# Kernel optimization log

Hardware: AMD Instinct MI355X
Metric: run time of the kernel (lower is better)

## Reference

```python
import jax, jax.numpy as jnp
from jax import lax
import numpy as np

H = 32  # hidden size (hardcoded by Linear(32,1) in the source)
I = 1   # input size

def setup_inputs() -> dict:
    key = jax.random.key(0)
    ks = jax.random.split(key, 8)
    B, T = 2048, 1024
    s_ih = 1.0 / np.sqrt(H)
    inp = {
        "x": jax.random.normal(ks[0], (B, T, I), dtype=jnp.float32),
        "h_state": jnp.zeros((1, B, H), dtype=jnp.float32),
        # GRU params, PyTorch layout: gates stacked as [r; z; n] -> [3H, *]
        "W_ih": jax.random.uniform(ks[1], (3 * H, I), jnp.float32, -s_ih, s_ih),
        "W_hh": jax.random.uniform(ks[2], (3 * H, H), jnp.float32, -s_ih, s_ih),
        "b_ih": jax.random.uniform(ks[3], (3 * H,), jnp.float32, -s_ih, s_ih),
        "b_hh": jax.random.uniform(ks[4], (3 * H,), jnp.float32, -s_ih, s_ih),
        # output Linear(32, 1)
        "W_out": jax.random.uniform(ks[5], (1, H), jnp.float32, -s_ih, s_ih),
        "b_out": jax.random.uniform(ks[6], (1,), jnp.float32, -s_ih, s_ih),
    }
    return inp

def _gru(x, h0, W_ih, W_hh, b_ih, b_hh):
    # Precompute input projections for all timesteps: [B,T,3H]
    x_proj = jnp.einsum('bti,gi->btg', x, W_ih) + b_ih
    xp_t = jnp.swapaxes(x_proj, 0, 1)  # [T,B,3H] for scan

    def step(h, xp):
        gh = h @ W_hh.T + b_hh  # [B,3H]
        r = jax.nn.sigmoid(xp[:, :H] + gh[:, :H])
        z = jax.nn.sigmoid(xp[:, H:2 * H] + gh[:, H:2 * H])
        n = jnp.tanh(xp[:, 2 * H:] + r * gh[:, 2 * H:])
        h_new = (1.0 - z) * n + z * h
        return h_new, h_new

    h_final, h_seq = lax.scan(step, h0[0], xp_t)
    return jnp.swapaxes(h_seq, 0, 1), h_final[None]  # [B,T,H], [1,B,H]

def reference(x, h_state, W_ih, W_hh, b_ih, b_hh, W_out, b_out):
    r_out, h_n = _gru(x, h_state, W_ih, W_hh, b_ih, b_hh)
    # per-timestep Linear(32,1), vectorized over time
    y = jnp.einsum('bth,oh->bto', r_out, W_out) + b_out  # [B,T,1]
    return (y, h_n)
```

## Files before the change

### kernel.cpp

```cpp
#include <hip/hip_runtime.h>


constexpr int H  = 32;
constexpr int TT = 1024;
constexpr int BB = 2048;

typedef _Float16 hf2 __attribute__((ext_vector_type(2)));

__device__ __forceinline__ unsigned pack2(float a, float b) {
    hf2 t; t.x = (_Float16)a; t.y = (_Float16)b;
    return __builtin_bit_cast(unsigned, t);
}

#define DOT48                                          \
    "v_dot2_f32_f16 v68, %[r0], v36, %[br]\n\t"        \
    "v_dot2_f32_f16 v69, %[z0], v36, %[bz]\n\t"        \
    "v_dot2_f32_f16 v70, %[n0], v36, %[bn]\n\t"        \
    "v_dot2_f32_f16 v68, %[r1], v37, v68\n\t"          \
    "v_dot2_f32_f16 v69, %[z1], v37, v69\n\t"          \
    "v_dot2_f32_f16 v70, %[n1], v37, v70\n\t"          \
    "v_dot2_f32_f16 v68, %[r2], v38, v68\n\t"          \
    "v_dot2_f32_f16 v69, %[z2], v38, v69\n\t"          \
    "v_dot2_f32_f16 v70, %[n2], v38, v70\n\t"          \
    "v_dot2_f32_f16 v68, %[r3], v39, v68\n\t"          \
    "v_dot2_f32_f16 v69, %[z3], v39, v69\n\t"          \
    "v_dot2_f32_f16 v70, %[n3], v39, v70\n\t"          \
    "v_dot2_f32_f16 v68, %[r4], v40, v68\n\t"          \
    "v_dot2_f32_f16 v69, %[z4], v40, v69\n\t"          \
    "v_dot2_f32_f16 v70, %[n4], v40, v70\n\t"          \
    "v_dot2_f32_f16 v68, %[r5], v41, v68\n\t"          \
    "v_dot2_f32_f16 v69, %[z5], v41, v69\n\t"          \
    "v_dot2_f32_f16 v70, %[n5], v41, v70\n\t"          \
    "v_dot2_f32_f16 v68, %[r6], v42, v68\n\t"          \
    "v_dot2_f32_f16 v69, %[z6], v42, v69\n\t"          \
    "v_dot2_f32_f16 v70, %[n6], v42, v70\n\t"          \
    "v_dot2_f32_f16 v68, %[r7], v43, v68\n\t"          \
    "v_dot2_f32_f16 v69, %[z7], v43, v69\n\t"          \
    "v_dot2_f32_f16 v70, %[n7], v43, v70\n\t"          \
    "v_dot2_f32_f16 v68, %[r8], v44, v68\n\t"          \
    "v_dot2_f32_f16 v69, %[z8], v44, v69\n\t"          \
    "v_dot2_f32_f16 v70, %[n8], v44, v70\n\t"          \
    "v_dot2_f32_f16 v68, %[r9], v45, v68\n\t"          \
    "v_dot2_f32_f16 v69, %[z9], v45, v69\n\t"          \
    "v_dot2_f32_f16 v70, %[n9], v45, v70\n\t"          \
    "v_dot2_f32_f16 v68, %[r10], v46, v68\n\t"         \
    "v_dot2_f32_f16 v69, %[z10], v46, v69\n\t"         \
    "v_dot2_f32_f16 v70, %[n10], v46, v70\n\t"         \
    "v_dot2_f32_f16 v68, %[r11], v47, v68\n\t"         \
    "v_dot2_f32_f16 v69, %[z11], v47, v69\n\t"         \
    "v_dot2_f32_f16 v70, %[n11], v47, v70\n\t"         \
    "v_dot2_f32_f16 v68, %[r12], v48, v68\n\t"         \
    "v_dot2_f32_f16 v69, %[z12], v48, v69\n\t"         \
    "v_dot2_f32_f16 v70, %[n12], v48, v70\n\t"         \
    "v_dot2_f32_f16 v68, %[r13], v49, v68\n\t"         \
    "v_dot2_f32_f16 v69, %[z13], v49, v69\n\t"         \
    "v_dot2_f32_f16 v70, %[n13], v49, v70\n\t"         \
    "v_dot2_f32_f16 v68, %[r14], v50, v68\n\t"         \
    "v_dot2_f32_f16 v69, %[z14], v50, v69\n\t"         \
    "v_dot2_f32_f16 v70, %[n14], v50, v70\n\t"         \
    "v_dot2_f32_f16 v68, %[r15], v51, v68\n\t"         \
    "v_dot2_f32_f16 v69, %[z15], v51, v69\n\t"         \
    "v_dot2_f32_f16 v70, %[n15], v51, v70\n\t"

#define TAIL(XREG, HREG)                               \
    "v_fmac_f32 v68, " XREG ", %[wir]\n\t"             \
    "v_fmac_f32 v69, " XREG ", %[wiz]\n\t"             \
    "v_exp_f32 v71, v68\n\t"                           \
    "v_exp_f32 v72, v69\n\t"                           \
    "v_fma_f32 v74, " XREG ", %[wi], %[bi]\n\t"        \
    "s_nop 3\n\t"                                      \
    "v_add_f32 v71, 1.0, v71\n\t"                      \
    "v_add_f32 v72, 1.0, v72\n\t"                      \
    "v_rcp_f32 v71, v71\n\t"                           \
    "v_rcp_f32 v72, v72\n\t"                           \
    "s_nop 3\n\t"                                      \
    "v_fmac_f32 v74, v71, v70\n\t"                     \
    "v_exp_f32 v75, v74\n\t"                           \
    "s_nop 3\n\t"                                      \
    "v_add_f32 v75, 1.0, v75\n\t"                      \
    "v_rcp_f32 v75, v75\n\t"                           \
    "s_nop 3\n\t"                                      \
    "v_fma_f32 v76, -2.0, v75, 1.0\n\t"                \
    "v_sub_f32 v77, " HREG ", v76\n\t"                 \
    "v_fma_f32 " HREG ", v72, v77, v76\n\t"

__global__ __launch_bounds__(256, 1)
void gru_fused(const float* __restrict__ x,
               const float* __restrict__ h0,
               const float* __restrict__ W_ih,
               const float* __restrict__ W_hh,
               const float* __restrict__ b_ih,
               const float* __restrict__ b_hh,
               const float* __restrict__ W_out,
               const float* __restrict__ b_out,
               float* __restrict__ out)
{
    __shared__ __align__(16) _Float16 hbuf[4][64];
    __shared__ __align__(8) float xstage[4][2][36];
    __shared__ float ybuf[4][2][33 * 32];

    const int tid  = threadIdx.x;
    const int w    = tid >> 6;
    const int lane = tid & 63;
    const int half = lane >> 5;
    const int j    = lane & 31;
    const int gw   = (blockIdx.x << 2) | w;
    const int b    = (gw << 1) | half;

    const float NL2E = -1.44269504f;
    const float P2L2 =  2.88539008f;

    const float* Wrp = &W_hh[(0 * H + j) * H];
    const float* Wzp = &W_hh[(1 * H + j) * H];
    const float* Wnp = &W_hh[(2 * H + j) * H];
    unsigned wr[16], wz[16], wn[16];
#pragma unroll
    for (int k = 0; k < 16; ++k) {
        wr[k] = pack2(Wrp[2 * k] * NL2E, Wrp[2 * k + 1] * NL2E);
        wz[k] = pack2(Wzp[2 * k] * NL2E, Wzp[2 * k + 1] * NL2E);
        wn[k] = pack2(Wnp[2 * k] * P2L2, Wnp[2 * k + 1] * P2L2);
    }
    const float wir = W_ih[j] * NL2E;
    const float wiz = W_ih[H + j] * NL2E;
    const float br  = (b_ih[j] + b_hh[j]) * NL2E;
    const float bz  = (b_ih[H + j] + b_hh[H + j]) * NL2E;
    const float bhn = b_hh[2 * H + j] * P2L2;
    const float win = W_ih[2 * H + j] * P2L2;
    const float bin = b_ih[2 * H + j] * P2L2;
    const float wo  = W_out[j];
    const float bo  = b_out[0];

    float h = h0[b * H + j];

    const float* xb = x + (size_t)b * TT;
    float*       yb = out + (size_t)b * TT;

    const unsigned ha = (unsigned)(size_t)&hbuf[w][half * 32 + j];
    const unsigned hr = (unsigned)(size_t)&hbuf[w][half * 32];
    const unsigned xw = (unsigned)(size_t)&xstage[w][half][j];
    const unsigned xa = (unsigned)(size_t)&xstage[w][half][0];
    const unsigned ya = (unsigned)(size_t)&ybuf[w][half][j];
    const float* yr = &ybuf[w][half][0];

#pragma unroll 1
    for (int t0 = 0; t0 < TT; t0 += 32) {
        const float xv = xb[t0 + j];

        asm volatile(
            "s_mov_b32 s20, 16\n\t"
            "v_mov_b32 v82, %[ya]\n\t"
            "v_mov_b32 v83, %[xa]\n\t"
            "ds_write_b32 %[xw], %[xv]\n\t"
            "ds_read_b64 v[80:81], v83\n\t"
            "v_cvt_f16_f32 v33, %[h]\n\t"
            "ds_write_b16 %[ha], v33\n\t"
            "ds_read_b128 v[36:39], %[hr]\n\t"
            "ds_read_b128 v[40:43], %[hr] offset:16\n\t"
            "ds_read_b128 v[44:47], %[hr] offset:32\n\t"
            "ds_read_b128 v[48:51], %[hr] offset:48\n\t"
            "ds_write_b32 v82, v78\n\t"

            "L_gru_%=:\n\t"
            "s_waitcnt lgkmcnt(1)\n\t"
            DOT48
            TAIL("v80", "%[h]")
            "v_cvt_f16_f32 v33, %[h]\n\t"
            "ds_write_b16 %[ha], v33\n\t"
            "ds_read_b128 v[36:39], %[hr]\n\t"
            "ds_read_b128 v[40:43], %[hr] offset:16\n\t"
            "ds_read_b128 v[44:47], %[hr] offset:32\n\t"
            "ds_read_b128 v[48:51], %[hr] offset:48\n\t"
            "v_mul_f32 v78, %[wo], %[h]\n\t"
            "ds_write_b32 v82, v78\n\t"
            "s_waitcnt lgkmcnt(1)\n\t"
            DOT48
            TAIL("v81", "%[h]")
            "v_cvt_f16_f32 v33, %[h]\n\t"
            "ds_write_b16 %[ha], v33\n\t"
            "ds_read_b128 v[36:39], %[hr]\n\t"
            "ds_read_b128 v[40:43], %[hr] offset:16\n\t"
            "ds_read_b128 v[44:47], %[hr] offset:32\n\t"
            "ds_read_b128 v[48:51], %[hr] offset:48\n\t"
            "ds_read_b64 v[80:81], v83 offset:8\n\t"
            "v_mul_f32 v78, %[wo], %[h]\n\t"
            "ds_write_b32 v82, v78 offset:132\n\t"
            "v_add_u32 v82, 264, v82\n\t"
            "v_add_u32 v83, 8, v83\n\t"
            "s_sub_i32 s20, s20, 1\n\t"
            "s_cmp_gt_i32 s20, 0\n\t"
            "s_cbranch_scc1 L_gru_%=\n\t"
            "s_waitcnt lgkmcnt(0)"
            : [h]"+v"(h)
            : [xv]"v"(xv), [ha]"v"(ha), [hr]"v"(hr), [xw]"v"(xw), [xa]"v"(xa),
              [ya]"v"(ya),
              [wir]"v"(wir), [wiz]"v"(wiz), [wi]"v"(win), [bi]"v"(bin),
              [wo]"v"(wo), [br]"v"(br), [bz]"v"(bz), [bn]"v"(bhn),
              [r0]"v"(wr[0]), [r1]"v"(wr[1]), [r2]"v"(wr[2]), [r3]"v"(wr[3]),
              [r4]"v"(wr[4]), [r5]"v"(wr[5]), [r6]"v"(wr[6]), [r7]"v"(wr[7]),
              [r8]"v"(wr[8]), [r9]"v"(wr[9]), [r10]"v"(wr[10]), [r11]"v"(wr[11]),
              [r12]"v"(wr[12]), [r13]"v"(wr[13]), [r14]"v"(wr[14]), [r15]"v"(wr[15]),
              [z0]"v"(wz[0]), [z1]"v"(wz[1]), [z2]"v"(wz[2]), [z3]"v"(wz[3]),
              [z4]"v"(wz[4]), [z5]"v"(wz[5]), [z6]"v"(wz[6]), [z7]"v"(wz[7]),
              [z8]"v"(wz[8]), [z9]"v"(wz[9]), [z10]"v"(wz[10]), [z11]"v"(wz[11]),
              [z12]"v"(wz[12]), [z13]"v"(wz[13]), [z14]"v"(wz[14]), [z15]"v"(wz[15]),
              [n0]"v"(wn[0]), [n1]"v"(wn[1]), [n2]"v"(wn[2]), [n3]"v"(wn[3]),
              [n4]"v"(wn[4]), [n5]"v"(wn[5]), [n6]"v"(wn[6]), [n7]"v"(wn[7]),
              [n8]"v"(wn[8]), [n9]"v"(wn[9]), [n10]"v"(wn[10]), [n11]"v"(wn[11]),
              [n12]"v"(wn[12]), [n13]"v"(wn[13]), [n14]"v"(wn[14]), [n15]"v"(wn[15])
            : "memory", "scc", "s20",
              "v33", "v36", "v37", "v38", "v39", "v40", "v41", "v42", "v43",
              "v44", "v45", "v46", "v47", "v48", "v49", "v50", "v51",
              "v68", "v69", "v70", "v71", "v72", "v74", "v75", "v76", "v77",
              "v78", "v80", "v81", "v82", "v83");

        float s0 = 0.0f, s1 = 0.0f, s2 = 0.0f, s3 = 0.0f;
#pragma unroll
        for (int k = 0; k < 32; k += 4) {
            s0 += yr[33 * j + k + 0];
            s1 += yr[33 * j + k + 1];
            s2 += yr[33 * j + k + 2];
            s3 += yr[33 * j + k + 3];
        }
        yb[t0 + j] = (s0 + s1) + (s2 + s3) + bo;
        __builtin_amdgcn_wave_barrier();
    }

    out[(size_t)BB * TT + b * H + j] = h;

#undef DOT48
#undef TAIL
}

extern "C" void kernel_launch(void* const* d_in, const int* in_sizes, int n_in,
                              void* d_out, int out_size, void* d_ws, size_t ws_size,
                              hipStream_t stream) {
    const float* x     = (const float*)d_in[0];
    const float* h0    = (const float*)d_in[1];
    const float* W_ih  = (const float*)d_in[2];
    const float* W_hh  = (const float*)d_in[3];
    const float* b_ih  = (const float*)d_in[4];
    const float* b_hh  = (const float*)d_in[5];
    const float* W_out = (const float*)d_in[6];
    const float* b_out = (const float*)d_in[7];
    float* out = (float*)d_out;

    dim3 grid(BB / 8);
    dim3 block(256);
    gru_fused<<<grid, block, 0, stream>>>(x, h0, W_ih, W_hh, b_ih, b_hh,
                                          W_out, b_out, out);
}
```

Measured before the change: 287.6 us.

## Broadcast hidden state via permlane16 swap and DPP butterflies instead of LDS

Each timestep's hidden-state exchange among the 32 lanes of a batch row used to go through an LDS write and four 128-bit LDS reads. It now uses v_permlane16_swap plus a set of DPP quad_perm and mirror moves to build the 16 packed f16 operands in registers. The W_hh weights are permuted per lane to match the butterfly ordering, and a runtime probe detects how the swap behaves. This removes LDS latency and waitcnt from the serial recurrence critical path, at the cost of many extra VALU moves and s_nop hazard stalls per step.

```diff
diff --git a/kernel.cpp b/kernel.cpp
--- a/kernel.cpp
+++ b/kernel.cpp
@@ -84,6 +84,34 @@
     "v_sub_f32 v77, " HREG ", v76\n\t"                 \
     "v_fma_f32 " HREG ", v72, v77, v76\n\t"
 
+#define BFLY(F1, F2)                                                        \
+    "v_cvt_f16_f32 v33, %[h]\n\t"                                           \
+    "v_mov_b32 v34, v33\n\t"                                                \
+    F1                                                                      \
+    "s_nop 1\n\t"                                                           \
+    "v_permlane16_swap_b32 v33, v34\n\t"                                    \
+    F2                                                                      \
+    "s_nop 1\n\t"                                                           \
+    "v_pack_b32_f16 v36, v33, v34\n\t"                                      \
+    "s_nop 1\n\t"                                                           \
+    "v_mov_b32 v37, v36 quad_perm:[1,0,3,2] row_mask:0xf bank_mask:0xf\n\t" \
+    "s_nop 1\n\t"                                                           \
+    "v_mov_b32 v38, v36 quad_perm:[2,3,0,1] row_mask:0xf bank_mask:0xf\n\t" \
+    "v_mov_b32 v39, v37 quad_perm:[2,3,0,1] row_mask:0xf bank_mask:0xf\n\t" \
+    "s_nop 1\n\t"                                                           \
+    "v_mov_b32 v40, v36 row_half_mirror row_mask:0xf bank_mask:0xf\n\t"     \
+    "v_mov_b32 v41, v37 row_half_mirror row_mask:0xf bank_mask:0xf\n\t"     \
+    "v_mov_b32 v42, v38 row_half_mirror row_mask:0xf bank_mask:0xf\n\t"     \
+    "v_mov_b32 v43, v39 row_half_mirror row_mask:0xf bank_mask:0xf\n\t"     \
+    "v_mov_b32 v44, v36 row_mirror row_mask:0xf bank_mask:0xf\n\t"          \
+    "v_mov_b32 v45, v37 row_mirror row_mask:0xf bank_mask:0xf\n\t"          \
+    "v_mov_b32 v46, v38 row_mirror row_mask:0xf bank_mask:0xf\n\t"          \
+    "v_mov_b32 v47, v39 row_mirror row_mask:0xf bank_mask:0xf\n\t"          \
+    "v_mov_b32 v48, v40 row_mirror row_mask:0xf bank_mask:0xf\n\t"          \
+    "v_mov_b32 v49, v41 row_mirror row_mask:0xf bank_mask:0xf\n\t"          \
+    "v_mov_b32 v50, v42 row_mirror row_mask:0xf bank_mask:0xf\n\t"          \
+    "v_mov_b32 v51, v43 row_mirror row_mask:0xf bank_mask:0xf\n\t"
+
 __global__ __launch_bounds__(256, 1)
 void gru_fused(const float* __restrict__ x,
                const float* __restrict__ h0,
@@ -95,7 +123,6 @@
                const float* __restrict__ b_out,
                float* __restrict__ out)
 {
-    __shared__ __align__(16) _Float16 hbuf[4][64];
     __shared__ __align__(8) float xstage[4][2][36];
     __shared__ float ybuf[4][2][33 * 32];
 
@@ -110,15 +137,29 @@
     const float NL2E = -1.44269504f;
     const float P2L2 =  2.88539008f;
 
+    int prb0 = (lane & 16) ? 1 : 0;
+    int prb1 = prb0;
+    asm volatile("s_nop 1\n\t"
+                 "v_permlane16_swap_b32 %0, %1\n\t"
+                 "s_nop 1"
+                 : "+v"(prb0), "+v"(prb1));
+    const bool swp = (prb0 != 0);
+
     const float* Wrp = &W_hh[(0 * H + j) * H];
     const float* Wzp = &W_hh[(1 * H + j) * H];
     const float* Wnp = &W_hh[(2 * H + j) * H];
+    const int c = j & 15;
+    const int M[16] = {0, 1, 2, 3, 7, 6, 5, 4, 15, 14, 13, 12, 8, 9, 10, 11};
     unsigned wr[16], wz[16], wn[16];
 #pragma unroll
-    for (int k = 0; k < 16; ++k) {
-        wr[k] = pack2(Wrp[2 * k] * NL2E, Wrp[2 * k + 1] * NL2E);
-        wz[k] = pack2(Wzp[2 * k] * NL2E, Wzp[2 * k + 1] * NL2E);
-        wn[k] = pack2(Wnp[2 * k] * P2L2, Wnp[2 * k + 1] * P2L2);
+    for (int r = 0; r < 16; ++r) {
+        const int k = c ^ M[r];
+        const float r0 = Wrp[k] * NL2E, r1 = Wrp[k + 16] * NL2E;
+        const float z0 = Wzp[k] * NL2E, z1 = Wzp[k + 16] * NL2E;
+        const float n0 = Wnp[k] * P2L2, n1 = Wnp[k + 16] * P2L2;
+        wr[r] = swp ? pack2(r1, r0) : pack2(r0, r1);
+        wz[r] = swp ? pack2(z1, z0) : pack2(z0, z1);
+        wn[r] = swp ? pack2(n1, n0) : pack2(n0, n1);
     }
     const float wir = W_ih[j] * NL2E;
     const float wiz = W_ih[H + j] * NL2E;
@@ -135,8 +176,6 @@
     const float* xb = x + (size_t)b * TT;
     float*       yb = out + (size_t)b * TT;
 
-    const unsigned ha = (unsigned)(size_t)&hbuf[w][half * 32 + j];
-    const unsigned hr = (unsigned)(size_t)&hbuf[w][half * 32];
     const unsigned xw = (unsigned)(size_t)&xstage[w][half][j];
     const unsigned xa = (unsigned)(size_t)&xstage[w][half][0];
     const unsigned ya = (unsigned)(size_t)&ybuf[w][half][j];
@@ -152,37 +191,19 @@
             "v_mov_b32 v83, %[xa]\n\t"
             "ds_write_b32 %[xw], %[xv]\n\t"
             "ds_read_b64 v[80:81], v83\n\t"
-            "v_cvt_f16_f32 v33, %[h]\n\t"
-            "ds_write_b16 %[ha], v33\n\t"
-            "ds_read_b128 v[36:39], %[hr]\n\t"
-            "ds_read_b128 v[40:43], %[hr] offset:16\n\t"
-            "ds_read_b128 v[44:47], %[hr] offset:32\n\t"
-            "ds_read_b128 v[48:51], %[hr] offset:48\n\t"
             "ds_write_b32 v82, v78\n\t"
+            BFLY("s_nop 1\n\t", "s_nop 1\n\t")
 
             "L_gru_%=:\n\t"
+            DOT48
             "s_waitcnt lgkmcnt(1)\n\t"
-            DOT48
             TAIL("v80", "%[h]")
-            "v_cvt_f16_f32 v33, %[h]\n\t"
-            "ds_write_b16 %[ha], v33\n\t"
-            "ds_read_b128 v[36:39], %[hr]\n\t"
-            "ds_read_b128 v[40:43], %[hr] offset:16\n\t"
-            "ds_read_b128 v[44:47], %[hr] offset:32\n\t"
-            "ds_read_b128 v[48:51], %[hr] offset:48\n\t"
-            "v_mul_f32 v78, %[wo], %[h]\n\t"
+            BFLY("v_mul_f32 v78, %[wo], %[h]\n\t", "s_nop 1\n\t")
             "ds_write_b32 v82, v78\n\t"
-            "s_waitcnt lgkmcnt(1)\n\t"
             DOT48
             TAIL("v81", "%[h]")
-            "v_cvt_f16_f32 v33, %[h]\n\t"
-            "ds_write_b16 %[ha], v33\n\t"
-            "ds_read_b128 v[36:39], %[hr]\n\t"
-            "ds_read_b128 v[40:43], %[hr] offset:16\n\t"
-            "ds_read_b128 v[44:47], %[hr] offset:32\n\t"
-            "ds_read_b128 v[48:51], %[hr] offset:48\n\t"
-            "ds_read_b64 v[80:81], v83 offset:8\n\t"
-            "v_mul_f32 v78, %[wo], %[h]\n\t"
+            BFLY("ds_read_b64 v[80:81], v83 offset:8\n\t",
+                 "v_mul_f32 v78, %[wo], %[h]\n\t")
             "ds_write_b32 v82, v78 offset:132\n\t"
             "v_add_u32 v82, 264, v82\n\t"
             "v_add_u32 v83, 8, v83\n\t"
@@ -191,8 +212,7 @@
             "s_cbranch_scc1 L_gru_%=\n\t"
             "s_waitcnt lgkmcnt(0)"
             : [h]"+v"(h)
-            : [xv]"v"(xv), [ha]"v"(ha), [hr]"v"(hr), [xw]"v"(xw), [xa]"v"(xa),
-              [ya]"v"(ya),
+            : [xv]"v"(xv), [xw]"v"(xw), [xa]"v"(xa), [ya]"v"(ya),
               [wir]"v"(wir), [wiz]"v"(wiz), [wi]"v"(win), [bi]"v"(bin),
               [wo]"v"(wo), [br]"v"(br), [bz]"v"(bz), [bn]"v"(bhn),
               [r0]"v"(wr[0]), [r1]"v"(wr[1]), [r2]"v"(wr[2]), [r3]"v"(wr[3]),
@@ -208,8 +228,8 @@
               [n8]"v"(wn[8]), [n9]"v"(wn[9]), [n10]"v"(wn[10]), [n11]"v"(wn[11]),
               [n12]"v"(wn[12]), [n13]"v"(wn[13]), [n14]"v"(wn[14]), [n15]"v"(wn[15])
             : "memory", "scc", "s20",
-              "v33", "v36", "v37", "v38", "v39", "v40", "v41", "v42", "v43",
-              "v44", "v45", "v46", "v47", "v48", "v49", "v50", "v51",
+              "v33", "v34", "v36", "v37", "v38", "v39", "v40", "v41", "v42",
+              "v43", "v44", "v45", "v46", "v47", "v48", "v49", "v50", "v51",
               "v68", "v69", "v70", "v71", "v72", "v74", "v75", "v76", "v77",
               "v78", "v80", "v81", "v82", "v83");
 
@@ -229,6 +249,7 @@
 
 #undef DOT48
 #undef TAIL
+#undef BFLY
 }
 
 extern "C" void kernel_launch(void* const* d_in, const int* in_sizes, int n_in,
```

Result: slower. 346.0 us (+20.3%).

## Split the hidden-dot across wave halves in fp32, combine with permlane32 swap

Applied to the files above, without the earlier changes.

Each wave now handles one batch row instead of two. Each 32-lane half computes half of the 32-wide recurrent dot product in fp32 FMAs, and the halves are combined with v_permlane32_swap. The fp16 packed dot2 and its conversions are dropped, the grid doubles, and launch bounds allow two blocks per CU. The aim is a shorter serial dependency chain per timestep and more waves in flight, at the cost of twice the waves and redundant tail math in both halves.

```diff
diff --git a/kernel.cpp b/kernel.cpp
--- a/kernel.cpp
+++ b/kernel.cpp
@@ -5,62 +5,68 @@
 constexpr int TT = 1024;
 constexpr int BB = 2048;
 
-typedef _Float16 hf2 __attribute__((ext_vector_type(2)));
-
-__device__ __forceinline__ unsigned pack2(float a, float b) {
-    hf2 t; t.x = (_Float16)a; t.y = (_Float16)b;
-    return __builtin_bit_cast(unsigned, t);
-}
-
-#define DOT48                                          \
-    "v_dot2_f32_f16 v68, %[r0], v36, %[br]\n\t"        \
-    "v_dot2_f32_f16 v69, %[z0], v36, %[bz]\n\t"        \
-    "v_dot2_f32_f16 v70, %[n0], v36, %[bn]\n\t"        \
-    "v_dot2_f32_f16 v68, %[r1], v37, v68\n\t"          \
-    "v_dot2_f32_f16 v69, %[z1], v37, v69\n\t"          \
-    "v_dot2_f32_f16 v70, %[n1], v37, v70\n\t"          \
-    "v_dot2_f32_f16 v68, %[r2], v38, v68\n\t"          \
-    "v_dot2_f32_f16 v69, %[z2], v38, v69\n\t"          \
-    "v_dot2_f32_f16 v70, %[n2], v38, v70\n\t"          \
-    "v_dot2_f32_f16 v68, %[r3], v39, v68\n\t"          \
-    "v_dot2_f32_f16 v69, %[z3], v39, v69\n\t"          \
-    "v_dot2_f32_f16 v70, %[n3], v39, v70\n\t"          \
-    "v_dot2_f32_f16 v68, %[r4], v40, v68\n\t"          \
-    "v_dot2_f32_f16 v69, %[z4], v40, v69\n\t"          \
-    "v_dot2_f32_f16 v70, %[n4], v40, v70\n\t"          \
-    "v_dot2_f32_f16 v68, %[r5], v41, v68\n\t"          \
-    "v_dot2_f32_f16 v69, %[z5], v41, v69\n\t"          \
-    "v_dot2_f32_f16 v70, %[n5], v41, v70\n\t"          \
-    "v_dot2_f32_f16 v68, %[r6], v42, v68\n\t"          \
-    "v_dot2_f32_f16 v69, %[z6], v42, v69\n\t"          \
-    "v_dot2_f32_f16 v70, %[n6], v42, v70\n\t"          \
-    "v_dot2_f32_f16 v68, %[r7], v43, v68\n\t"          \
-    "v_dot2_f32_f16 v69, %[z7], v43, v69\n\t"          \
-    "v_dot2_f32_f16 v70, %[n7], v43, v70\n\t"          \
-    "v_dot2_f32_f16 v68, %[r8], v44, v68\n\t"          \
-    "v_dot2_f32_f16 v69, %[z8], v44, v69\n\t"          \
-    "v_dot2_f32_f16 v70, %[n8], v44, v70\n\t"          \
-    "v_dot2_f32_f16 v68, %[r9], v45, v68\n\t"          \
-    "v_dot2_f32_f16 v69, %[z9], v45, v69\n\t"          \
-    "v_dot2_f32_f16 v70, %[n9], v45, v70\n\t"          \
-    "v_dot2_f32_f16 v68, %[r10], v46, v68\n\t"         \
-    "v_dot2_f32_f16 v69, %[z10], v46, v69\n\t"         \
-    "v_dot2_f32_f16 v70, %[n10], v46, v70\n\t"         \
-    "v_dot2_f32_f16 v68, %[r11], v47, v68\n\t"         \
-    "v_dot2_f32_f16 v69, %[z11], v47, v69\n\t"         \
-    "v_dot2_f32_f16 v70, %[n11], v47, v70\n\t"         \
-    "v_dot2_f32_f16 v68, %[r12], v48, v68\n\t"         \
-    "v_dot2_f32_f16 v69, %[z12], v48, v69\n\t"         \
-    "v_dot2_f32_f16 v70, %[n12], v48, v70\n\t"         \
-    "v_dot2_f32_f16 v68, %[r13], v49, v68\n\t"         \
-    "v_dot2_f32_f16 v69, %[z13], v49, v69\n\t"         \
-    "v_dot2_f32_f16 v70, %[n13], v49, v70\n\t"         \
-    "v_dot2_f32_f16 v68, %[r14], v50, v68\n\t"         \
-    "v_dot2_f32_f16 v69, %[z14], v50, v69\n\t"         \
-    "v_dot2_f32_f16 v70, %[n14], v50, v70\n\t"         \
-    "v_dot2_f32_f16 v68, %[r15], v51, v68\n\t"         \
-    "v_dot2_f32_f16 v69, %[z15], v51, v69\n\t"         \
-    "v_dot2_f32_f16 v70, %[n15], v51, v70\n\t"
+#define DOT48F                                         \
+    "v_fma_f32 v68, %[r0], v36, %[br]\n\t"             \
+    "v_fma_f32 v69, %[z0], v36, %[bz]\n\t"             \
+    "v_fma_f32 v70, %[n0], v36, %[bn]\n\t"             \
+    "v_fmac_f32 v68, %[r1], v37\n\t"                   \
+    "v_fmac_f32 v69, %[z1], v37\n\t"                   \
+    "v_fmac_f32 v70, %[n1], v37\n\t"                   \
+    "v_fmac_f32 v68, %[r2], v38\n\t"                   \
+    "v_fmac_f32 v69, %[z2], v38\n\t"                   \
+    "v_fmac_f32 v70, %[n2], v38\n\t"                   \
+    "v_fmac_f32 v68, %[r3], v39\n\t"                   \
+    "v_fmac_f32 v69, %[z3], v39\n\t"                   \
+    "v_fmac_f32 v70, %[n3], v39\n\t"                   \
+    "v_fmac_f32 v68, %[r4], v40\n\t"                   \
+    "v_fmac_f32 v69, %[z4], v40\n\t"                   \
+    "v_fmac_f32 v70, %[n4], v40\n\t"                   \
+    "v_fmac_f32 v68, %[r5], v41\n\t"                   \
+    "v_fmac_f32 v69, %[z5], v41\n\t"                   \
+    "v_fmac_f32 v70, %[n5], v41\n\t"                   \
+    "v_fmac_f32 v68, %[r6], v42\n\t"                   \
+    "v_fmac_f32 v69, %[z6], v42\n\t"                   \
+    "v_fmac_f32 v70, %[n6], v42\n\t"                   \
+    "v_fmac_f32 v68, %[r7], v43\n\t"                   \
+    "v_fmac_f32 v69, %[z7], v43\n\t"                   \
+    "v_fmac_f32 v70, %[n7], v43\n\t"                   \
+    "v_fmac_f32 v68, %[r8], v44\n\t"                   \
+    "v_fmac_f32 v69, %[z8], v44\n\t"                   \
+    "v_fmac_f32 v70, %[n8], v44\n\t"                   \
+    "v_fmac_f32 v68, %[r9], v45\n\t"                   \
+    "v_fmac_f32 v69, %[z9], v45\n\t"                   \
+    "v_fmac_f32 v70, %[n9], v45\n\t"                   \
+    "v_fmac_f32 v68, %[r10], v46\n\t"                  \
+    "v_fmac_f32 v69, %[z10], v46\n\t"                  \
+    "v_fmac_f32 v70, %[n10], v46\n\t"                  \
+    "v_fmac_f32 v68, %[r11], v47\n\t"                  \
+    "v_fmac_f32 v69, %[z11], v47\n\t"                  \
+    "v_fmac_f32 v70, %[n11], v47\n\t"                  \
+    "v_fmac_f32 v68, %[r12], v48\n\t"                  \
+    "v_fmac_f32 v69, %[z12], v48\n\t"                  \
+    "v_fmac_f32 v70, %[n12], v48\n\t"                  \
+    "v_fmac_f32 v68, %[r13], v49\n\t"                  \
+    "v_fmac_f32 v69, %[z13], v49\n\t"                  \
+    "v_fmac_f32 v70, %[n13], v49\n\t"                  \
+    "v_fmac_f32 v68, %[r14], v50\n\t"                  \
+    "v_fmac_f32 v69, %[z14], v50\n\t"                  \
+    "v_fmac_f32 v70, %[n14], v50\n\t"                  \
+    "v_fmac_f32 v68, %[r15], v51\n\t"                  \
+    "v_fmac_f32 v69, %[z15], v51\n\t"                  \
+    "v_fmac_f32 v70, %[n15], v51\n\t"
+
+#define COMBINE                                        \
+    "v_mov_b32 v64, v68\n\t"                           \
+    "v_mov_b32 v65, v69\n\t"                           \
+    "v_mov_b32 v66, v70\n\t"                           \
+    "s_nop 1\n\t"                                      \
+    "v_permlane32_swap_b32 v64, v68\n\t"               \
+    "v_permlane32_swap_b32 v65, v69\n\t"               \
+    "v_permlane32_swap_b32 v66, v70\n\t"               \
+    "s_nop 1\n\t"                                      \
+    "v_add_f32 v68, v64, v68\n\t"                      \
+    "v_add_f32 v69, v65, v69\n\t"                      \
+    "v_add_f32 v70, v66, v70\n\t"
 
 #define TAIL(XREG, HREG)                               \
     "v_fmac_f32 v68, " XREG ", %[wir]\n\t"             \
@@ -84,7 +90,7 @@
     "v_sub_f32 v77, " HREG ", v76\n\t"                 \
     "v_fma_f32 " HREG ", v72, v77, v76\n\t"
 
-__global__ __launch_bounds__(256, 1)
+__global__ __launch_bounds__(256, 2)
 void gru_fused(const float* __restrict__ x,
                const float* __restrict__ h0,
                const float* __restrict__ W_ih,
@@ -95,7 +101,7 @@
                const float* __restrict__ b_out,
                float* __restrict__ out)
 {
-    __shared__ __align__(16) _Float16 hbuf[4][64];
+    __shared__ __align__(64) float hbuf[4][2][32];
     __shared__ __align__(8) float xstage[4][2][36];
     __shared__ float ybuf[4][2][33 * 32];
 
@@ -104,8 +110,7 @@
     const int lane = tid & 63;
     const int half = lane >> 5;
     const int j    = lane & 31;
-    const int gw   = (blockIdx.x << 2) | w;
-    const int b    = (gw << 1) | half;
+    const int b    = (blockIdx.x << 2) | w;
 
     const float NL2E = -1.44269504f;
     const float P2L2 =  2.88539008f;
@@ -113,18 +118,19 @@
     const float* Wrp = &W_hh[(0 * H + j) * H];
     const float* Wzp = &W_hh[(1 * H + j) * H];
     const float* Wnp = &W_hh[(2 * H + j) * H];
-    unsigned wr[16], wz[16], wn[16];
+    const int kb = 16 * half;
+    float wr[16], wz[16], wn[16];
 #pragma unroll
-    for (int k = 0; k < 16; ++k) {
-        wr[k] = pack2(Wrp[2 * k] * NL2E, Wrp[2 * k + 1] * NL2E);
-        wz[k] = pack2(Wzp[2 * k] * NL2E, Wzp[2 * k + 1] * NL2E);
-        wn[k] = pack2(Wnp[2 * k] * P2L2, Wnp[2 * k + 1] * P2L2);
+    for (int p = 0; p < 16; ++p) {
+        wr[p] = Wrp[kb + p] * NL2E;
+        wz[p] = Wzp[kb + p] * NL2E;
+        wn[p] = Wnp[kb + p] * P2L2;
     }
+    const float br  = half ? 0.0f : (b_ih[j] + b_hh[j]) * NL2E;
+    const float bz  = half ? 0.0f : (b_ih[H + j] + b_hh[H + j]) * NL2E;
+    const float bhn = half ? 0.0f : b_hh[2 * H + j] * P2L2;
     const float wir = W_ih[j] * NL2E;
     const float wiz = W_ih[H + j] * NL2E;
-    const float br  = (b_ih[j] + b_hh[j]) * NL2E;
-    const float bz  = (b_ih[H + j] + b_hh[H + j]) * NL2E;
-    const float bhn = b_hh[2 * H + j] * P2L2;
     const float win = W_ih[2 * H + j] * P2L2;
     const float bin = b_ih[2 * H + j] * P2L2;
     const float wo  = W_out[j];
@@ -135,8 +141,8 @@
     const float* xb = x + (size_t)b * TT;
     float*       yb = out + (size_t)b * TT;
 
-    const unsigned ha = (unsigned)(size_t)&hbuf[w][half * 32 + j];
-    const unsigned hr = (unsigned)(size_t)&hbuf[w][half * 32];
+    const unsigned ha = (unsigned)(size_t)&hbuf[w][half][j];
+    const unsigned hr = (unsigned)(size_t)&hbuf[w][half][16 * half];
     const unsigned xw = (unsigned)(size_t)&xstage[w][half][j];
     const unsigned xa = (unsigned)(size_t)&xstage[w][half][0];
     const unsigned ya = (unsigned)(size_t)&ybuf[w][half][j];
@@ -152,8 +158,7 @@
             "v_mov_b32 v83, %[xa]\n\t"
             "ds_write_b32 %[xw], %[xv]\n\t"
             "ds_read_b64 v[80:81], v83\n\t"
-            "v_cvt_f16_f32 v33, %[h]\n\t"
-            "ds_write_b16 %[ha], v33\n\t"
+            "ds_write_b32 %[ha], %[h]\n\t"
             "ds_read_b128 v[36:39], %[hr]\n\t"
             "ds_read_b128 v[40:43], %[hr] offset:16\n\t"
             "ds_read_b128 v[44:47], %[hr] offset:32\n\t"
@@ -162,10 +167,10 @@
 
             "L_gru_%=:\n\t"
             "s_waitcnt lgkmcnt(1)\n\t"
-            DOT48
+            DOT48F
+            COMBINE
             TAIL("v80", "%[h]")
-            "v_cvt_f16_f32 v33, %[h]\n\t"
-            "ds_write_b16 %[ha], v33\n\t"
+            "ds_write_b32 %[ha], %[h]\n\t"
             "ds_read_b128 v[36:39], %[hr]\n\t"
             "ds_read_b128 v[40:43], %[hr] offset:16\n\t"
             "ds_read_b128 v[44:47], %[hr] offset:32\n\t"
@@ -173,10 +178,10 @@
             "v_mul_f32 v78, %[wo], %[h]\n\t"
             "ds_write_b32 v82, v78\n\t"
             "s_waitcnt lgkmcnt(1)\n\t"
-            DOT48
+            DOT48F
+            COMBINE
             TAIL("v81", "%[h]")
-            "v_cvt_f16_f32 v33, %[h]\n\t"
-            "ds_write_b16 %[ha], v33\n\t"
+            "ds_write_b32 %[ha], %[h]\n\t"
             "ds_read_b128 v[36:39], %[hr]\n\t"
             "ds_read_b128 v[40:43], %[hr] offset:16\n\t"
             "ds_read_b128 v[44:47], %[hr] offset:32\n\t"
@@ -208,8 +213,9 @@
               [n8]"v"(wn[8]), [n9]"v"(wn[9]), [n10]"v"(wn[10]), [n11]"v"(wn[11]),
               [n12]"v"(wn[12]), [n13]"v"(wn[13]), [n14]"v"(wn[14]), [n15]"v"(wn[15])
             : "memory", "scc", "s20",
-              "v33", "v36", "v37", "v38", "v39", "v40", "v41", "v42", "v43",
+              "v36", "v37", "v38", "v39", "v40", "v41", "v42", "v43",
               "v44", "v45", "v46", "v47", "v48", "v49", "v50", "v51",
+              "v64", "v65", "v66",
               "v68", "v69", "v70", "v71", "v72", "v74", "v75", "v76", "v77",
               "v78", "v80", "v81", "v82", "v83");
 
@@ -221,13 +227,14 @@
             s2 += yr[33 * j + k + 2];
             s3 += yr[33 * j + k + 3];
         }
-        yb[t0 + j] = (s0 + s1) + (s2 + s3) + bo;
+        if (!half) yb[t0 + j] = (s0 + s1) + (s2 + s3) + bo;
         __builtin_amdgcn_wave_barrier();
     }
 
-    out[(size_t)BB * TT + b * H + j] = h;
-
-#undef DOT48
+    if (!half) out[(size_t)BB * TT + b * H + j] = h;
+
+#undef DOT48F
+#undef COMBINE
 #undef TAIL
 }
 
@@ -244,7 +251,7 @@
     const float* b_out = (const float*)d_in[7];
     float* out = (float*)d_out;
 
-    dim3 grid(BB / 8);
+    dim3 grid(BB / 4);
     dim3 block(256);
     gru_fused<<<grid, block, 0, stream>>>(x, h0, W_ih, W_hh, b_ih, b_hh,
                                           W_out, b_out, out);
```

Result: slower. 394.1 us (+37.1%).

## Overlap LDS reads with dot chain and hoist input projection off critical path

Applied to the files above, without the earlier changes.

Splits the 48-instruction dot-product block into four groups, each gated by its own lgkmcnt wait, so compute on the first hidden-state chunk starts before all four LDS reads land. The input-projection FMAs (x*W_ir+b_r, x*W_iz+b_z) are precomputed into spare registers and used as the dot-chain accumulator seeds, taking them out of the serial recurrence. Loop bookkeeping and the next x read are moved into former s_nop slots. The z*h and (1-z) terms are computed early so the final update is one FMA. The gain depends on the hand-placed waitcnts being correct and on the shorter s_nop padding still meeting hazard requirements.

```diff
diff --git a/kernel.cpp b/kernel.cpp
--- a/kernel.cpp
+++ b/kernel.cpp
@@ -12,9 +12,9 @@
     return __builtin_bit_cast(unsigned, t);
 }
 
-#define DOT48                                          \
-    "v_dot2_f32_f16 v68, %[r0], v36, %[br]\n\t"        \
-    "v_dot2_f32_f16 v69, %[z0], v36, %[bz]\n\t"        \
+#define DOT12_0(SR, SZ)                                \
+    "v_dot2_f32_f16 v68, %[r0], v36, " SR "\n\t"       \
+    "v_dot2_f32_f16 v69, %[z0], v36, " SZ "\n\t"       \
     "v_dot2_f32_f16 v70, %[n0], v36, %[bn]\n\t"        \
     "v_dot2_f32_f16 v68, %[r1], v37, v68\n\t"          \
     "v_dot2_f32_f16 v69, %[z1], v37, v69\n\t"          \
@@ -24,7 +24,9 @@
     "v_dot2_f32_f16 v70, %[n2], v38, v70\n\t"          \
     "v_dot2_f32_f16 v68, %[r3], v39, v68\n\t"          \
     "v_dot2_f32_f16 v69, %[z3], v39, v69\n\t"          \
-    "v_dot2_f32_f16 v70, %[n3], v39, v70\n\t"          \
+    "v_dot2_f32_f16 v70, %[n3], v39, v70\n\t"
+
+#define DOT12_1                                        \
     "v_dot2_f32_f16 v68, %[r4], v40, v68\n\t"          \
     "v_dot2_f32_f16 v69, %[z4], v40, v69\n\t"          \
     "v_dot2_f32_f16 v70, %[n4], v40, v70\n\t"          \
@@ -36,7 +38,9 @@
     "v_dot2_f32_f16 v70, %[n6], v42, v70\n\t"          \
     "v_dot2_f32_f16 v68, %[r7], v43, v68\n\t"          \
     "v_dot2_f32_f16 v69, %[z7], v43, v69\n\t"          \
-    "v_dot2_f32_f16 v70, %[n7], v43, v70\n\t"          \
+    "v_dot2_f32_f16 v70, %[n7], v43, v70\n\t"
+
+#define DOT12_2                                        \
     "v_dot2_f32_f16 v68, %[r8], v44, v68\n\t"          \
     "v_dot2_f32_f16 v69, %[z8], v44, v69\n\t"          \
     "v_dot2_f32_f16 v70, %[n8], v44, v70\n\t"          \
@@ -48,7 +52,9 @@
     "v_dot2_f32_f16 v70, %[n10], v46, v70\n\t"         \
     "v_dot2_f32_f16 v68, %[r11], v47, v68\n\t"         \
     "v_dot2_f32_f16 v69, %[z11], v47, v69\n\t"         \
-    "v_dot2_f32_f16 v70, %[n11], v47, v70\n\t"         \
+    "v_dot2_f32_f16 v70, %[n11], v47, v70\n\t"
+
+#define DOT12_3                                        \
     "v_dot2_f32_f16 v68, %[r12], v48, v68\n\t"         \
     "v_dot2_f32_f16 v69, %[z12], v48, v69\n\t"         \
     "v_dot2_f32_f16 v70, %[n12], v48, v70\n\t"         \
@@ -62,27 +68,39 @@
     "v_dot2_f32_f16 v69, %[z15], v51, v69\n\t"         \
     "v_dot2_f32_f16 v70, %[n15], v51, v70\n\t"
 
-#define TAIL(XREG, HREG)                               \
-    "v_fmac_f32 v68, " XREG ", %[wir]\n\t"             \
-    "v_fmac_f32 v69, " XREG ", %[wiz]\n\t"             \
+#define DOT48G(SR, SZ)                                 \
+    "s_waitcnt lgkmcnt(4)\n\t"                         \
+    DOT12_0(SR, SZ)                                    \
+    "s_waitcnt lgkmcnt(3)\n\t"                         \
+    DOT12_1                                            \
+    "s_waitcnt lgkmcnt(2)\n\t"                         \
+    DOT12_2                                            \
+    "s_waitcnt lgkmcnt(1)\n\t"                         \
+    DOT12_3
+
+#define TAIL(XREG, F1, F2, SLOT4)                      \
     "v_exp_f32 v71, v68\n\t"                           \
     "v_exp_f32 v72, v69\n\t"                           \
     "v_fma_f32 v74, " XREG ", %[wi], %[bi]\n\t"        \
-    "s_nop 3\n\t"                                      \
+    F1                                                 \
+    "s_nop 1\n\t"                                      \
     "v_add_f32 v71, 1.0, v71\n\t"                      \
     "v_add_f32 v72, 1.0, v72\n\t"                      \
     "v_rcp_f32 v71, v71\n\t"                           \
     "v_rcp_f32 v72, v72\n\t"                           \
-    "s_nop 3\n\t"                                      \
+    F2                                                 \
+    "s_nop 1\n\t"                                      \
     "v_fmac_f32 v74, v71, v70\n\t"                     \
+    "v_mul_f32 v79, v72, %[h]\n\t"                     \
+    "v_sub_f32 v73, 1.0, v72\n\t"                      \
     "v_exp_f32 v75, v74\n\t"                           \
     "s_nop 3\n\t"                                      \
     "v_add_f32 v75, 1.0, v75\n\t"                      \
     "v_rcp_f32 v75, v75\n\t"                           \
-    "s_nop 3\n\t"                                      \
+    SLOT4                                              \
     "v_fma_f32 v76, -2.0, v75, 1.0\n\t"                \
-    "v_sub_f32 v77, " HREG ", v76\n\t"                 \
-    "v_fma_f32 " HREG ", v72, v77, v76\n\t"
+    "v_fma_f32 %[h], v73, v76, v79\n\t"                \
+    "v_cvt_f16_f32 v33, %[h]\n\t"
 
 __global__ __launch_bounds__(256, 1)
 void gru_fused(const float* __restrict__ x,
@@ -159,12 +177,16 @@
             "ds_read_b128 v[44:47], %[hr] offset:32\n\t"
             "ds_read_b128 v[48:51], %[hr] offset:48\n\t"
             "ds_write_b32 v82, v78\n\t"
+            "s_waitcnt lgkmcnt(6)\n\t"
+            "v_fma_f32 v84, v80, %[wir], %[br]\n\t"
+            "v_fma_f32 v85, v80, %[wiz], %[bz]\n\t"
 
             "L_gru_%=:\n\t"
-            "s_waitcnt lgkmcnt(1)\n\t"
-            DOT48
-            TAIL("v80", "%[h]")
-            "v_cvt_f16_f32 v33, %[h]\n\t"
+            DOT48G("v84", "v85")
+            TAIL("v80",
+                 "v_fma_f32 v86, v81, %[wir], %[br]\n\t",
+                 "v_fma_f32 v87, v81, %[wiz], %[bz]\n\t",
+                 "s_nop 3\n\t")
             "ds_write_b16 %[ha], v33\n\t"
             "ds_read_b128 v[36:39], %[hr]\n\t"
             "ds_read_b128 v[40:43], %[hr] offset:16\n\t"
@@ -172,22 +194,24 @@
             "ds_read_b128 v[48:51], %[hr] offset:48\n\t"
             "v_mul_f32 v78, %[wo], %[h]\n\t"
             "ds_write_b32 v82, v78\n\t"
-            "s_waitcnt lgkmcnt(1)\n\t"
-            DOT48
-            TAIL("v81", "%[h]")
-            "v_cvt_f16_f32 v33, %[h]\n\t"
+            DOT48G("v86", "v87")
+            TAIL("v81",
+                 "v_add_u32 v83, 8, v83\n\t",
+                 "ds_read_b64 v[80:81], v83\n\t",
+                 "s_sub_i32 s20, s20, 1\n\t"
+                 "s_cmp_gt_i32 s20, 0\n\t"
+                 "s_nop 1\n\t")
             "ds_write_b16 %[ha], v33\n\t"
             "ds_read_b128 v[36:39], %[hr]\n\t"
             "ds_read_b128 v[40:43], %[hr] offset:16\n\t"
             "ds_read_b128 v[44:47], %[hr] offset:32\n\t"
             "ds_read_b128 v[48:51], %[hr] offset:48\n\t"
-            "ds_read_b64 v[80:81], v83 offset:8\n\t"
             "v_mul_f32 v78, %[wo], %[h]\n\t"
             "ds_write_b32 v82, v78 offset:132\n\t"
+            "s_waitcnt lgkmcnt(6)\n\t"
+            "v_fma_f32 v84, v80, %[wir], %[br]\n\t"
+            "v_fma_f32 v85, v80, %[wiz], %[bz]\n\t"
             "v_add_u32 v82, 264, v82\n\t"
-            "v_add_u32 v83, 8, v83\n\t"
-            "s_sub_i32 s20, s20, 1\n\t"
-            "s_cmp_gt_i32 s20, 0\n\t"
             "s_cbranch_scc1 L_gru_%=\n\t"
             "s_waitcnt lgkmcnt(0)"
             : [h]"+v"(h)
@@ -210,8 +234,9 @@
             : "memory", "scc", "s20",
               "v33", "v36", "v37", "v38", "v39", "v40", "v41", "v42", "v43",
               "v44", "v45", "v46", "v47", "v48", "v49", "v50", "v51",
-              "v68", "v69", "v70", "v71", "v72", "v74", "v75", "v76", "v77",
-              "v78", "v80", "v81", "v82", "v83");
+              "v68", "v69", "v70", "v71", "v72", "v73", "v74", "v75", "v76",
+              "v78", "v79", "v80", "v81", "v82", "v83", "v84", "v85", "v86",
+              "v87");
 
         float s0 = 0.0f, s1 = 0.0f, s2 = 0.0f, s3 = 0.0f;
 #pragma unroll
@@ -227,7 +252,11 @@
 
     out[(size_t)BB * TT + b * H + j] = h;
 
-#undef DOT48
+#undef DOT12_0
+#undef DOT12_1
+#undef DOT12_2
+#undef DOT12_3
+#undef DOT48G
 #undef TAIL
 }
 
```

Measured after the change: 290.3 us. No clear change (+0.9%).
